# Performance work log

Measured on AMD Instinct MI355X. Metric: run time of the kernel, lower is better.

## Reference

```python
import jax, jax.numpy as jnp
import numpy as np
from jax import lax

B, T, V, E, H = 256, 16, 32000, 256, 512


def setup_inputs() -> dict:
    key = jax.random.key(0)
    ks = jax.random.split(key, 10)
    s = 0.02
    return {
        "x": jax.random.normal(ks[0], (B, E), dtype=jnp.float32),
        "bb_w": jax.random.normal(ks[1], (H, E), dtype=jnp.float32) * s,
        "bb_b": jnp.zeros((H,), jnp.float32),
        "ln_g": jnp.ones((H,), jnp.float32),
        "ln_b": jnp.zeros((H,), jnp.float32),
        "emb": jax.random.normal(ks[2], (V, E), dtype=jnp.float32) * s,
        "sos": jax.random.normal(ks[3], (E,), dtype=jnp.float32) * 0.01,
        "wih0": jax.random.normal(ks[4], (4 * H, E), dtype=jnp.float32) * s,
        "whh0": jax.random.normal(ks[5], (4 * H, H), dtype=jnp.float32) * s,
        "bih0": jnp.zeros((4 * H,), jnp.float32),
        "bhh0": jnp.zeros((4 * H,), jnp.float32),
        "wih1": jax.random.normal(ks[6], (4 * H, H), dtype=jnp.float32) * s,
        "whh1": jax.random.normal(ks[7], (4 * H, H), dtype=jnp.float32) * s,
        "bih1": jnp.zeros((4 * H,), jnp.float32),
        "bhh1": jnp.zeros((4 * H,), jnp.float32),
        "out_w": jax.random.normal(ks[8], (V, H), dtype=jnp.float32) * s,
        "out_b": jnp.zeros((V,), jnp.float32),
    }


def _lstm_cell(x, h, c, wih, whh, bih, bhh):
    # PyTorch LSTMCell gate order: input, forget, cell(g), output
    g = x @ wih.T + bih + h @ whh.T + bhh
    i, f, gg, o = jnp.split(g, 4, axis=-1)
    c2 = jax.nn.sigmoid(f) * c + jax.nn.sigmoid(i) * jnp.tanh(gg)
    h2 = jax.nn.sigmoid(o) * jnp.tanh(c2)
    return h2, c2


def reference(x, bb_w, bb_b, ln_g, ln_b, emb, sos, wih0, whh0, bih0, bhh0,
              wih1, whh1, bih1, bhh1, out_w, out_b):
    # backbone: Linear -> LayerNorm -> GELU (exact erf, torch default)
    z = x @ bb_w.T + bb_b
    mu = z.mean(-1, keepdims=True)
    var = ((z - mu) ** 2).mean(-1, keepdims=True)
    z = (z - mu) / jnp.sqrt(var + 1e-5) * ln_g + ln_b
    h0 = jax.nn.gelu(z, approximate=False)

    keys = jax.random.split(jax.random.key(1), T)
    init = (
        jnp.broadcast_to(sos[None, :], (B, E)),  # inp
        h0, jnp.zeros_like(h0),                  # layer 0 h, c
        jnp.zeros_like(h0), jnp.zeros_like(h0),  # layer 1 h, c
        jnp.zeros((B,), jnp.bool_),              # done
    )

    def step(carry, key):
        inp, h0_, c0_, h1_, c1_, done = carry
        h0_, c0_ = _lstm_cell(inp, h0_, c0_, wih0, whh0, bih0, bhh0)
        h1_, c1_ = _lstm_cell(h0_, h1_, c1_, wih1, whh1, bih1, bhh1)
        logits = (h1_ @ out_w.T + out_b).astype(jnp.float32)  # [B, V]
        tok = jax.random.categorical(key, logits)
        logl = jax.nn.log_softmax(logits)
        logp = jnp.take_along_axis(logl, tok[:, None], axis=1)[:, 0]
        ent = -jnp.sum(jnp.exp(logl) * logl, axis=-1)
        # varlen masking
        tok = jnp.where(done, 0, tok)
        logp = jnp.where(done, 0.0, logp)
        ent = jnp.where(done, 0.0, ent)
        done = done | (tok == 0)
        inp = emb[tok]
        return (inp, h0_, c0_, h1_, c1_, done), (tok, logp, ent)

    _, (ids, logp, ent) = lax.scan(step, init, keys)
    ids = ids.T          # [B, T]
    logp = logp.T
    ent = ent.T

    # find_lengths_eos + zero ids from (lengths-1) onward
    eos = ids == 0
    has_eos = eos.any(axis=1)
    first = jnp.argmax(eos, axis=1)
    lengths = jnp.where(has_eos, first + 1, T)
    t = jnp.arange(T)[None, :]
    after = t >= (lengths - 1)[:, None]
    ids = jnp.where(after, 0, ids)
    msg = jax.nn.one_hot(ids, V, dtype=jnp.float32)  # [B, T, V]
    return ids, msg, logp, ent, lengths
```

## Files before the change

### kernel.cpp

```cpp
#include <hip/hip_runtime.h>
#include <cstdint>
#include <cmath>

#define B_ 256
#define T_ 16
#define V_ 32000
#define E_ 256
#define H_ 512

typedef __attribute__((ext_vector_type(8))) short bf16x8;
typedef __attribute__((ext_vector_type(4))) float f32x4;

__device__ __forceinline__ uint32_t rotl32(uint32_t x, int r) {
  return (x << r) | (x >> (32 - r));
}

__device__ __forceinline__ void tf2x32(uint32_t k0, uint32_t k1, uint32_t x0, uint32_t x1,
                                       uint32_t& o0, uint32_t& o1) {
  uint32_t k2 = k0 ^ k1 ^ 0x1BD11BDAu;
  x0 += k0; x1 += k1;
#define TFR(r) { x0 += x1; x1 = rotl32(x1, (r)); x1 ^= x0; }
  TFR(13) TFR(15) TFR(26) TFR(6)   x0 += k1; x1 += k2 + 1u;
  TFR(17) TFR(29) TFR(16) TFR(24)  x0 += k2; x1 += k0 + 2u;
  TFR(13) TFR(15) TFR(26) TFR(6)   x0 += k0; x1 += k1 + 3u;
  TFR(17) TFR(29) TFR(16) TFR(24)  x0 += k1; x1 += k2 + 4u;
  TFR(13) TFR(15) TFR(26) TFR(6)   x0 += k2; x1 += k0 + 5u;
#undef TFR
  o0 = x0; o1 = x1;
}

__device__ __forceinline__ uint32_t f2bf(float x) {
  uint32_t u = __float_as_uint(x);
  return (u + 0x7fffu + ((u >> 16) & 1u)) >> 16;
}

typedef const __attribute__((address_space(1))) void* as1_t;
typedef __attribute__((address_space(3))) void* as3_t;
__device__ __forceinline__ void glds16(const void* g, void* l) {
  __builtin_amdgcn_global_load_lds((as1_t)g, (as3_t)l, 16, 0, 0);
}

__global__ __launch_bounds__(256) void prep_all(
    const float* __restrict__ wih0, const float* __restrict__ whh0,
    const float* __restrict__ bih0, const float* __restrict__ bhh0,
    const float* __restrict__ wih1, const float* __restrict__ whh1,
    const float* __restrict__ bih1, const float* __restrict__ bhh1,
    const float* __restrict__ out_w,
    ushort* __restrict__ W30, ushort* __restrict__ W31,
    float* __restrict__ bq0, float* __restrict__ bq1,
    ushort* __restrict__ B2, uint32_t* __restrict__ keys)
{
  const long long stride = (long long)gridDim.x * blockDim.x;
  const long long i0 = (long long)blockIdx.x * blockDim.x + threadIdx.x;
  if (i0 < 16) {
    uint32_t o0, o1;
    tf2x32(0u, 1u, 0u, (uint32_t)i0, o0, o1);
    keys[2 * i0] = o0; keys[2 * i0 + 1] = o1;
  }
  const long long S0 = 2048LL * 768;
  const long long T1 = S0;
  const long long T2 = T1 + 2048LL * 1024;
  const long long T3 = T2 + 2048;
  const long long T4 = T3 + 2048;
  const long long T5 = T4 + 32000LL * 512;
  for (long long i = i0; i < T5; i += stride) {
    if (i < T1) {
      int n = (int)(i / 768), k = (int)(i % 768);
      int r = (n & 3) * 512 + (n >> 2);
      float x = (k < 256) ? wih0[(size_t)r * 256 + k] : whh0[(size_t)r * 512 + (k - 256)];
      uint32_t hi = f2bf(x);
      float hf = __uint_as_float(hi << 16);
      uint32_t lo = f2bf(x - hf);
      ushort* row = W30 + (size_t)n * 1536;
      row[k] = (ushort)hi; row[768 + k] = (ushort)lo;
    } else if (i < T2) {
      long long q = i - T1;
      int n = (int)(q / 1024), k = (int)(q % 1024);
      int r = (n & 3) * 512 + (n >> 2);
      float x = (k < 512) ? wih1[(size_t)r * 512 + k] : whh1[(size_t)r * 512 + (k - 512)];
      uint32_t hi = f2bf(x);
      float hf = __uint_as_float(hi << 16);
      uint32_t lo = f2bf(x - hf);
      ushort* row = W31 + (size_t)n * 2048;
      row[k] = (ushort)hi; row[1024 + k] = (ushort)lo;
    } else if (i < T3) {
      int n = (int)(i - T2);
      int r = (n & 3) * 512 + (n >> 2);
      bq0[n] = bih0[r] + bhh0[r];
    } else if (i < T4) {
      int n = (int)(i - T3);
      int r = (n & 3) * 512 + (n >> 2);
      bq1[n] = bih1[r] + bhh1[r];
    } else {
      long long q = i - T4;
      int n = (int)(q >> 9), k = (int)(q & 511);
      float x = out_w[q];
      uint32_t hi = f2bf(x);
      float hf = __uint_as_float(hi << 16);
      uint32_t lo = f2bf(x - hf);
      ushort* row = B2 + (size_t)n * 1024;
      row[k] = (ushort)hi; row[512 + k] = (ushort)lo;
    }
  }
}

__global__ __launch_bounds__(256) void backbone_kernel(
    const float* __restrict__ x, const float* __restrict__ bb_w, const float* __restrict__ bb_b,
    const float* __restrict__ ln_g, const float* __restrict__ ln_b, const float* __restrict__ sos,
    ushort* __restrict__ A0a, ushort* __restrict__ A1a,
    float* __restrict__ c0, float* __restrict__ c1, int* __restrict__ done)
{
  const int b = blockIdx.x, tid = threadIdx.x;
  __shared__ float xs[E_];
  __shared__ float zs[H_];
  __shared__ float red[256];
  xs[tid] = x[b * E_ + tid];
  __syncthreads();
  for (int jj = 0; jj < 2; ++jj) {
    int j = jj * 256 + tid;
    float acc = 0.0f;
#pragma unroll 4
    for (int k = 0; k < E_; ++k) acc = fmaf(xs[k], bb_w[(size_t)j * E_ + k], acc);
    zs[j] = acc + bb_b[j];
  }
  __syncthreads();
  red[tid] = zs[tid] + zs[tid + 256];
  __syncthreads();
  for (int off = 128; off > 0; off >>= 1) { if (tid < off) red[tid] += red[tid + off]; __syncthreads(); }
  const float mu = red[0] / 512.0f;
  __syncthreads();
  {
    float d0 = zs[tid] - mu, d1 = zs[tid + 256] - mu;
    red[tid] = d0 * d0 + d1 * d1;
  }
  __syncthreads();
  for (int off = 128; off > 0; off >>= 1) { if (tid < off) red[tid] += red[tid + off]; __syncthreads(); }
  const float var = red[0] / 512.0f;
  const float sv = sqrtf(var + 1e-5f);
  for (int jj = 0; jj < 2; ++jj) {
    int j = jj * 256 + tid;
    float zn = (zs[j] - mu) / sv * ln_g[j] + ln_b[j];
    float h = 0.5f * zn * (1.0f + erff(zn / 1.41421356237309515f));
    uint32_t hi = f2bf(h);
    float hf = __uint_as_float(hi << 16);
    uint32_t lo = f2bf(h - hf);
    A0a[(size_t)b * 1536 + 256 + j]  = (ushort)hi;
    A0a[(size_t)b * 1536 + 1024 + j] = (ushort)lo;
    A1a[(size_t)b * 2048 + 512 + j]  = 0;
    A1a[(size_t)b * 2048 + 1536 + j] = 0;
    c0[(size_t)b * 512 + j] = 0.0f;
    c1[(size_t)b * 512 + j] = 0.0f;
  }
  {
    const float xv = sos[tid];
    uint32_t hi = f2bf(xv);
    float hf = __uint_as_float(hi << 16);
    uint32_t lo = f2bf(xv - hf);
    A0a[(size_t)b * 1536 + tid]       = (ushort)hi;
    A0a[(size_t)b * 1536 + 768 + tid] = (ushort)lo;
  }
  if (tid == 0) done[b] = 0;
}

template<int TK>
__global__ __launch_bounds__(256) void mfma_lstm(
    const ushort* __restrict__ A3, const ushort* __restrict__ W3,
    const float* __restrict__ bias, float* __restrict__ c,
    ushort* __restrict__ d1, int rs1, int o1h, int o1l,
    ushort* __restrict__ d2, int rs2, int o2h, int o2l)
{
  constexpr int K = TK * 64;
  constexpr int KC = 3 * TK;
  constexpr int NR = KC / 4;
  constexpr int RS = 2 * K;
  __shared__ __align__(16) char smem[98304];
  const int tid = threadIdx.x;
  const int lane = tid & 63;
  const int wid = tid >> 6;
  const int wm = wid >> 1, wn = wid & 1;
  const int m0 = blockIdx.y * 32;
  const int n0 = blockIdx.x * 64;

  auto stage_chunk = [&](int kc, char* cbase) {
    const int tI = kc / TK;
    const int kin = kc - tI * TK;
    const int abase = (tI == 2 ? K : 0) + kin * 64;
    const int wbase = (tI == 1 ? K : 0) + kin * 64;
    {
      const int o = wid * 1024 + lane * 16;
      const int row = o >> 7;
      const int kb = (o >> 4) & 7;
      glds16(A3 + (size_t)(m0 + row) * RS + abase + ((kb ^ (row & 7)) << 3),
             (void*)(cbase + wid * 1024));
    }
#pragma unroll
    for (int s = 0; s < 2; ++s) {
      const int o = (wid * 2 + s) * 1024 + lane * 16;
      const int row = o >> 7;
      const int kb = (o >> 4) & 7;
      glds16(W3 + (size_t)(n0 + row) * RS + wbase + ((kb ^ (row & 7)) << 3),
             (void*)(cbase + 4096 + (wid * 2 + s) * 1024));
    }
  };
  auto stage_round = [&](int r, char* base) {
#pragma unroll
    for (int cch = 0; cch < 4; ++cch) stage_chunk(r * 4 + cch, base + cch * 12288);
  };

  f32x4 acc[2];
#pragma unroll
  for (int j = 0; j < 2; ++j)
#pragma unroll
    for (int q = 0; q < 4; ++q) acc[j][q] = 0.0f;

  stage_round(0, smem);
  asm volatile("s_waitcnt vmcnt(0)" ::: "memory");
  __syncthreads();
  for (int r = 0; r < NR; ++r) {
    char* cur = smem + (r & 1) * 49152;
    if (r + 1 < NR) stage_round(r + 1, smem + ((r + 1) & 1) * 49152);
#pragma unroll
    for (int cch = 0; cch < 4; ++cch) {
      char* lds = cur + cch * 12288;
#pragma unroll
      for (int ks = 0; ks < 2; ++ks) {
        const int kb = ks * 4 + (lane >> 4);
        const int arow = wm * 16 + (lane & 15);
        bf16x8 a = *(const bf16x8*)(lds + arow * 128 + ((kb ^ (arow & 7)) << 4));
        bf16x8 w[2];
#pragma unroll
        for (int j = 0; j < 2; ++j) {
          const int col = wn * 32 + j * 16 + (lane & 15);
          w[j] = *(const bf16x8*)(lds + 4096 + col * 128 + ((kb ^ (col & 7)) << 4));
        }
#pragma unroll
        for (int j = 0; j < 2; ++j)
          acc[j] = __builtin_amdgcn_mfma_f32_16x16x32_bf16(a, w[j], acc[j], 0, 0, 0);
      }
    }
    asm volatile("s_waitcnt vmcnt(0)" ::: "memory");
    __syncthreads();
  }
  float* gls = (float*)smem;
#pragma unroll
  for (int j = 0; j < 2; ++j)
#pragma unroll
    for (int q = 0; q < 4; ++q)
      gls[(wm * 16 + (lane >> 4) * 4 + q) * 65 + wn * 32 + j * 16 + (lane & 15)] = acc[j][q];
  __syncthreads();
  const int row = tid >> 3;
  const int m = m0 + row;
#pragma unroll
  for (int e = 0; e < 2; ++e) {
    const int ul = (tid & 7) * 2 + e;
    const int nc = ul * 4;
    const float gi = gls[row * 65 + nc + 0] + bias[n0 + nc + 0];
    const float gf = gls[row * 65 + nc + 1] + bias[n0 + nc + 1];
    const float gg = gls[row * 65 + nc + 2] + bias[n0 + nc + 2];
    const float go = gls[row * 65 + nc + 3] + bias[n0 + nc + 3];
    const int u = (n0 >> 2) + ul;
    const float si = 1.0f / (1.0f + expf(-gi));
    const float sf = 1.0f / (1.0f + expf(-gf));
    const float so = 1.0f / (1.0f + expf(-go));
    const float cn = sf * c[(size_t)m * 512 + u] + si * tanhf(gg);
    const float hn = so * tanhf(cn);
    c[(size_t)m * 512 + u] = cn;
    const uint32_t hi = f2bf(hn);
    const float hf = __uint_as_float(hi << 16);
    const uint32_t lo = f2bf(hn - hf);
    d1[(size_t)m * rs1 + o1h + u] = (ushort)hi;
    d1[(size_t)m * rs1 + o1l + u] = (ushort)lo;
    d2[(size_t)m * rs2 + o2h + u] = (ushort)hi;
    d2[(size_t)m * rs2 + o2l + u] = (ushort)lo;
  }
}

__global__ __launch_bounds__(512) void mfma_logits(
    const ushort* __restrict__ A2,
    const ushort* __restrict__ B2,
    const float* __restrict__ bias,
    float* __restrict__ logits)
{
  __shared__ __align__(16) char smem[65536];
  char* lds = smem;
  const int tid = threadIdx.x;
  const int lane = tid & 63;
  const int wid = tid >> 6;
  const int wm = wid >> 2, wn = wid & 3;
  const int bid = blockIdx.x;
  const int xcd = bid & 7, idx = bid >> 3;
  const int wg = (xcd < 4 ? xcd * 63 : 252 + (xcd - 4) * 62) + idx;
  const int m0 = (wg & 1) * 128;
  const int n0 = (wg >> 1) * 128;

  auto stage = [&](int kc, int base) {
    const int tI = kc >> 3;
    const int kin = kc & 7;
    const int abase = (tI == 2 ? 512 : 0) + kin * 64;
    const int bbase = (tI == 1 ? 512 : 0) + kin * 64;
#pragma unroll
    for (int s = 0; s < 2; ++s) {
      const int o = (wid * 2 + s) * 1024 + lane * 16;
      const int row = o >> 7;
      const int kb = (o >> 4) & 7;
      const int sw = (kb ^ (row & 7)) << 3;
      glds16(A2 + (size_t)(m0 + row) * 1024 + abase + sw,
             (void*)(lds + base + (wid * 2 + s) * 1024));
      glds16(B2 + (size_t)(n0 + row) * 1024 + bbase + sw,
             (void*)(lds + base + 16384 + (wid * 2 + s) * 1024));
    }
  };

  f32x4 acc[4][2];
#pragma unroll
  for (int i = 0; i < 4; ++i)
#pragma unroll
    for (int j = 0; j < 2; ++j)
#pragma unroll
      for (int q = 0; q < 4; ++q) acc[i][j][q] = 0.0f;

  stage(0, 0);
  asm volatile("s_waitcnt vmcnt(0)" ::: "memory");
  __syncthreads();
  for (int kc = 0; kc < 24; ++kc) {
    const int cb = (kc & 1) * 32768;
    if (kc + 1 < 24) stage(kc + 1, cb ^ 32768);
#pragma unroll
    for (int ks = 0; ks < 2; ++ks) {
      bf16x8 a[4], b[2];
      const int kb = ks * 4 + (lane >> 4);
#pragma unroll
      for (int i = 0; i < 4; ++i) {
        const int row = wm * 64 + i * 16 + (lane & 15);
        a[i] = *(const bf16x8*)(lds + cb + row * 128 + ((kb ^ (row & 7)) << 4));
      }
#pragma unroll
      for (int j = 0; j < 2; ++j) {
        const int col = wn * 32 + j * 16 + (lane & 15);
        b[j] = *(const bf16x8*)(lds + cb + 16384 + col * 128 + ((kb ^ (col & 7)) << 4));
      }
#pragma unroll
      for (int i = 0; i < 4; ++i)
#pragma unroll
        for (int j = 0; j < 2; ++j)
          acc[i][j] = __builtin_amdgcn_mfma_f32_16x16x32_bf16(a[i], b[j], acc[i][j], 0, 0, 0);
    }
    asm volatile("s_waitcnt vmcnt(0)" ::: "memory");
    __syncthreads();
  }
  const int lsub = lane & 15;
  float bj[2];
#pragma unroll
  for (int j = 0; j < 2; ++j) bj[j] = bias[n0 + wn * 32 + j * 16 + lsub];
  const int rbase = (lane >> 4) * 4;
#pragma unroll
  for (int i = 0; i < 4; ++i) {
    const int m = m0 + wm * 64 + i * 16 + rbase;
#pragma unroll
    for (int j = 0; j < 2; ++j) {
      const int n = n0 + wn * 32 + j * 16 + lsub;
#pragma unroll
      for (int q = 0; q < 4; ++q)
        logits[(size_t)(m + q) * V_ + n] = acc[i][j][q] + bj[j];
    }
  }
}

__global__ __launch_bounds__(512) void sample_row(
    const float* __restrict__ logits, const uint32_t* __restrict__ keys, int t,
    const float* __restrict__ emb, int* __restrict__ done,
    ushort* __restrict__ A0next, float* __restrict__ ids,
    float* __restrict__ logp, float* __restrict__ ent, float* __restrict__ lens)
{
  const int b = blockIdx.x, tid = threadIdx.x;
  const uint32_t k0 = keys[2 * t], k1 = keys[2 * t + 1];
  const float* lrow = logits + (size_t)b * V_;

  float S = 0.0f, Aa = 0.0f, sb = -INFINITY, lb = 0.0f; int ib = 0;
  float th = -INFINITY;
  int it = 0;
  for (int idx = tid; idx < V_ / 4; idx += 512, ++it) {
    float4 l4 = *(const float4*)&lrow[idx * 4];
    const float le[4] = {l4.x, l4.y, l4.z, l4.w};
#pragma unroll
    for (int e = 0; e < 4; ++e) {
      const int v = idx * 4 + e;
      uint32_t o0, o1;
      tf2x32(k0, k1, 0u, (uint32_t)(b * V_ + v), o0, o1);
      const uint32_t man = (o0 ^ o1) >> 9;
      const float u = (man == 0u) ? 1.17549435e-38f
                                  : __uint_as_float(man | 0x3f800000u) - 1.0f;
      const float ex = expf(le[e]);
      S += ex; Aa = fmaf(ex, le[e], Aa);
      const float thl = fmaxf(th, sb);
      bool need = true;
      if (thl > -1e30f) {
        const float uth = __expf(-__expf(-(thl - le[e] - 1e-3f)));
        need = (u >= uth);
      }
      if (need) {
        const float inner = (float)log((double)u);
        const float outer = (float)log((double)(-inner));
        const float s = le[e] - outer;
        if (s > sb) { sb = s; ib = v; lb = le[e]; }
      }
    }
    if (it == 0 || it == 3) {
      float m2 = sb;
#pragma unroll
      for (int o = 1; o < 64; o <<= 1) m2 = fmaxf(m2, __shfl_xor(m2, o));
      th = m2;
    }
  }
  __shared__ float ss[512], sa[512], sv[512], sl[512];
  __shared__ int si[512];
  ss[tid] = S; sa[tid] = Aa; sv[tid] = sb; si[tid] = ib; sl[tid] = lb;
  __syncthreads();
  for (int o = 256; o > 0; o >>= 1) {
    if (tid < o) {
      ss[tid] += ss[tid + o]; sa[tid] += sa[tid + o];
      float v2 = sv[tid + o]; int i2 = si[tid + o];
      if (v2 > sv[tid] || (v2 == sv[tid] && i2 < si[tid])) {
        sv[tid] = v2; si[tid] = i2; sl[tid] = sl[tid + o];
      }
    }
    __syncthreads();
  }
  if (tid == 0) {
    const float Ssum = ss[0], Asum = sa[0];
    const float logS = logf(Ssum);
    const int tok = si[0];
    const float lp = sl[0] - logS;
    const float en = logS - Asum / Ssum;
    const int dn = done[b];
    const int tokm = dn ? 0 : tok;
    ids[b * T_ + t]  = (float)tokm;
    logp[b * T_ + t] = dn ? 0.0f : lp;
    ent[b * T_ + t]  = dn ? 0.0f : en;
    done[b] = dn | (tokm == 0);
    si[0] = tokm;
    if (t == T_ - 1) {
      int len = T_; bool has = false;
      for (int tt = 0; tt < T_; ++tt) {
        if (!has && ids[b * T_ + tt] == 0.0f) { has = true; len = tt + 1; }
      }
      for (int tt = len - 1; tt < T_; ++tt) ids[b * T_ + tt] = 0.0f;
      lens[b] = (float)len;
    }
  }
  __syncthreads();
  const int tk = si[0];
  if (tid < E_) {
    const float xv = emb[(size_t)tk * E_ + tid];
    const uint32_t hi = f2bf(xv);
    const float hf = __uint_as_float(hi << 16);
    const uint32_t lo = f2bf(xv - hf);
    A0next[(size_t)b * 1536 + tid]       = (ushort)hi;
    A0next[(size_t)b * 1536 + 768 + tid] = (ushort)lo;
  }
}

__global__ __launch_bounds__(256) void msg_kernel(const float* __restrict__ ids,
                                                  float* __restrict__ msg) {
  const int bt = blockIdx.x;
  const int id = (int)ids[bt];
  float4* dst = (float4*)(msg + (size_t)bt * V_);
  for (int q = threadIdx.x; q < V_ / 4; q += 256) {
    const int v = q * 4;
    float4 val;
    val.x = (v     == id) ? 1.0f : 0.0f;
    val.y = (v + 1 == id) ? 1.0f : 0.0f;
    val.z = (v + 2 == id) ? 1.0f : 0.0f;
    val.w = (v + 3 == id) ? 1.0f : 0.0f;
    dst[q] = val;
  }
}

extern "C" void kernel_launch(void* const* d_in, const int* in_sizes, int n_in,
                              void* d_out, int out_size, void* d_ws, size_t ws_size,
                              hipStream_t stream) {
  const float* x    = (const float*)d_in[0];
  const float* bb_w = (const float*)d_in[1];
  const float* bb_b = (const float*)d_in[2];
  const float* ln_g = (const float*)d_in[3];
  const float* ln_b = (const float*)d_in[4];
  const float* emb  = (const float*)d_in[5];
  const float* sos  = (const float*)d_in[6];
  const float* wih0 = (const float*)d_in[7];
  const float* whh0 = (const float*)d_in[8];
  const float* bih0 = (const float*)d_in[9];
  const float* bhh0 = (const float*)d_in[10];
  const float* wih1 = (const float*)d_in[11];
  const float* whh1 = (const float*)d_in[12];
  const float* bih1 = (const float*)d_in[13];
  const float* bhh1 = (const float*)d_in[14];
  const float* out_w = (const float*)d_in[15];
  const float* out_b = (const float*)d_in[16];

  float* out  = (float*)d_out;
  float* ids  = out;
  float* msg  = out + 4096;
  float* logp = out + 131076096;
  float* ent  = out + 131080192;
  float* lens = out + 131084288;

  float* p = msg;
  ushort* W30 = (ushort*)p; p += 1572864;
  ushort* W31 = (ushort*)p; p += 2097152;
  float* bq0 = p; p += 2048;
  float* bq1 = p; p += 2048;
  ushort* A0a = (ushort*)p; p += 196608;
  ushort* A0b = (ushort*)p; p += 196608;
  ushort* A1a = (ushort*)p; p += 262144;
  ushort* A1b = (ushort*)p; p += 262144;
  float* c0 = p; p += 131072;
  float* c1 = p; p += 131072;
  ushort* A2 = (ushort*)p; p += 131072;
  ushort* B2 = (ushort*)p; p += 16384000;
  float* logits = p; p += 8192000;
  uint32_t* keys = (uint32_t*)p; p += 64;
  int* done = (int*)p; p += 256;

  prep_all<<<4096, 256, 0, stream>>>(wih0, whh0, bih0, bhh0,
                                     wih1, whh1, bih1, bhh1, out_w,
                                     W30, W31, bq0, bq1, B2, keys);
  backbone_kernel<<<256, 256, 0, stream>>>(x, bb_w, bb_b, ln_g, ln_b, sos,
                                           A0a, A1a, c0, c1, done);
  for (int t = 0; t < T_; ++t) {
    ushort* A0c = (t & 1) ? A0b : A0a;
    ushort* A0n = (t & 1) ? A0a : A0b;
    ushort* A1c = (t & 1) ? A1b : A1a;
    ushort* A1n = (t & 1) ? A1a : A1b;
    mfma_lstm<12><<<dim3(32, 8), 256, 0, stream>>>(
        A0c, W30, bq0, c0,
        A1c, 2048, 0, 1024,
        A0n, 1536, 256, 1024);
    mfma_lstm<16><<<dim3(32, 8), 256, 0, stream>>>(
        A1c, W31, bq1, c1,
        A1n, 2048, 512, 1536,
        A2, 1024, 0, 512);
    mfma_logits<<<500, 512, 0, stream>>>(A2, B2, out_b, logits);
    sample_row<<<256, 512, 0, stream>>>(logits, keys, t, emb, done,
                                        A0n, ids, logp, ent, lens);
  }
  msg_kernel<<<4096, 256, 0, stream>>>(ids, msg);
}
```

Measured before the change: 1.787 ms.

## Deepen LDS prefetch pipelines in LSTM and logits GEMM kernels

```diff
diff --git a/kernel.cpp b/kernel.cpp
--- a/kernel.cpp
+++ b/kernel.cpp
@@ -57,8 +57,7 @@
     tf2x32(0u, 1u, 0u, (uint32_t)i0, o0, o1);
     keys[2 * i0] = o0; keys[2 * i0 + 1] = o1;
   }
-  const long long S0 = 2048LL * 768;
-  const long long T1 = S0;
+  const long long T1 = 2048LL * 768;
   const long long T2 = T1 + 2048LL * 1024;
   const long long T3 = T2 + 2048;
   const long long T4 = T3 + 2048;
@@ -173,7 +172,7 @@
   constexpr int KC = 3 * TK;
   constexpr int NR = KC / 4;
   constexpr int RS = 2 * K;
-  __shared__ __align__(16) char smem[98304];
+  __shared__ __align__(16) char smem[147456];
   const int tid = threadIdx.x;
   const int lane = tid & 63;
   const int wid = tid >> 6;
@@ -202,7 +201,8 @@
              (void*)(cbase + 4096 + (wid * 2 + s) * 1024));
     }
   };
-  auto stage_round = [&](int r, char* base) {
+  auto stage_round = [&](int r) {
+    char* base = smem + (r % 3) * 49152;
 #pragma unroll
     for (int cch = 0; cch < 4; ++cch) stage_chunk(r * 4 + cch, base + cch * 12288);
   };
@@ -213,12 +213,13 @@
 #pragma unroll
     for (int q = 0; q < 4; ++q) acc[j][q] = 0.0f;
 
-  stage_round(0, smem);
-  asm volatile("s_waitcnt vmcnt(0)" ::: "memory");
+  stage_round(0);
+  stage_round(1);
+  asm volatile("s_waitcnt vmcnt(12)" ::: "memory");
   __syncthreads();
   for (int r = 0; r < NR; ++r) {
-    char* cur = smem + (r & 1) * 49152;
-    if (r + 1 < NR) stage_round(r + 1, smem + ((r + 1) & 1) * 49152);
+    char* cur = smem + (r % 3) * 49152;
+    if (r + 2 < NR) stage_round(r + 2);
 #pragma unroll
     for (int cch = 0; cch < 4; ++cch) {
       char* lds = cur + cch * 12288;
@@ -238,7 +239,8 @@
           acc[j] = __builtin_amdgcn_mfma_f32_16x16x32_bf16(a, w[j], acc[j], 0, 0, 0);
       }
     }
-    asm volatile("s_waitcnt vmcnt(0)" ::: "memory");
+    if (r + 2 < NR) asm volatile("s_waitcnt vmcnt(12)" ::: "memory");
+    else            asm volatile("s_waitcnt vmcnt(0)" ::: "memory");
     __syncthreads();
   }
   float* gls = (float*)smem;
@@ -281,8 +283,7 @@
     const float* __restrict__ bias,
     float* __restrict__ logits)
 {
-  __shared__ __align__(16) char smem[65536];
-  char* lds = smem;
+  __shared__ __align__(16) char smem[131072];
   const int tid = threadIdx.x;
   const int lane = tid & 63;
   const int wid = tid >> 6;
@@ -293,7 +294,8 @@
   const int m0 = (wg & 1) * 128;
   const int n0 = (wg >> 1) * 128;
 
-  auto stage = [&](int kc, int base) {
+  auto stage = [&](int kc) {
+    char* base = smem + (kc & 3) * 32768;
     const int tI = kc >> 3;
     const int kin = kc & 7;
     const int abase = (tI == 2 ? 512 : 0) + kin * 64;
@@ -305,9 +307,9 @@
       const int kb = (o >> 4) & 7;
       const int sw = (kb ^ (row & 7)) << 3;
       glds16(A2 + (size_t)(m0 + row) * 1024 + abase + sw,
-             (void*)(lds + base + (wid * 2 + s) * 1024));
+             (void*)(base + (wid * 2 + s) * 1024));
       glds16(B2 + (size_t)(n0 + row) * 1024 + bbase + sw,
-             (void*)(lds + base + 16384 + (wid * 2 + s) * 1024));
+             (void*)(base + 16384 + (wid * 2 + s) * 1024));
     }
   };
 
@@ -319,12 +321,12 @@
 #pragma unroll
       for (int q = 0; q < 4; ++q) acc[i][j][q] = 0.0f;
 
-  stage(0, 0);
-  asm volatile("s_waitcnt vmcnt(0)" ::: "memory");
+  stage(0); stage(1); stage(2);
+  asm volatile("s_waitcnt vmcnt(8)" ::: "memory");
   __syncthreads();
   for (int kc = 0; kc < 24; ++kc) {
-    const int cb = (kc & 1) * 32768;
-    if (kc + 1 < 24) stage(kc + 1, cb ^ 32768);
+    char* lds = smem + (kc & 3) * 32768;
+    if (kc + 3 < 24) stage(kc + 3);
 #pragma unroll
     for (int ks = 0; ks < 2; ++ks) {
       bf16x8 a[4], b[2];
@@ -332,12 +334,12 @@
 #pragma unroll
       for (int i = 0; i < 4; ++i) {
         const int row = wm * 64 + i * 16 + (lane & 15);
-        a[i] = *(const bf16x8*)(lds + cb + row * 128 + ((kb ^ (row & 7)) << 4));
+        a[i] = *(const bf16x8*)(lds + row * 128 + ((kb ^ (row & 7)) << 4));
       }
 #pragma unroll
       for (int j = 0; j < 2; ++j) {
         const int col = wn * 32 + j * 16 + (lane & 15);
-        b[j] = *(const bf16x8*)(lds + cb + 16384 + col * 128 + ((kb ^ (col & 7)) << 4));
+        b[j] = *(const bf16x8*)(lds + 16384 + col * 128 + ((kb ^ (col & 7)) << 4));
       }
 #pragma unroll
       for (int i = 0; i < 4; ++i)
@@ -345,7 +347,9 @@
         for (int j = 0; j < 2; ++j)
           acc[i][j] = __builtin_amdgcn_mfma_f32_16x16x32_bf16(a[i], b[j], acc[i][j], 0, 0, 0);
     }
-    asm volatile("s_waitcnt vmcnt(0)" ::: "memory");
+    if (kc + 3 < 24)      asm volatile("s_waitcnt vmcnt(8)" ::: "memory");
+    else if (kc + 2 < 24) asm volatile("s_waitcnt vmcnt(4)" ::: "memory");
+    else                  asm volatile("s_waitcnt vmcnt(0)" ::: "memory");
     __syncthreads();
   }
   const int lsub = lane & 15;
```

Result: slower. 1.868 ms (+4.5%).
